# Optimization experiments

Measured on AMD Instinct MI355X. Metric: run time of the kernel, lower is better.

The kernel has to match this reference:

```python
import jax, jax.numpy as jnp
import numpy as np

N = 100000   # nodes
E = 1600000  # edges
D = 128      # feature dim
G = 64       # graphs in batch


def setup_inputs() -> dict:
    key = jax.random.key(0)
    k1, k2, k3, k4, k5, k6, k7, k8 = jax.random.split(key, 8)
    in_feat = jax.random.normal(k1, (N, D), dtype=jnp.float32)
    src = jax.random.randint(k2, (E,), 0, N, dtype=jnp.int32)
    dst = jax.random.randint(k3, (E,), 0, N, dtype=jnp.int32)
    graph_ids = jax.random.randint(k4, (N,), 0, G, dtype=jnp.int32)
    s = 1.0 / np.sqrt(D)
    W1 = jax.random.uniform(k5, (D, D), jnp.float32, -s, s)
    b1 = jnp.zeros((D,), jnp.float32)
    W2 = jax.random.uniform(k6, (D, D), jnp.float32, -s, s)
    b2 = jnp.zeros((D,), jnp.float32)
    return {"in_feat": in_feat, "W1": W1, "b1": b1, "W2": W2, "b2": b2,
            "src": src, "dst": dst, "graph_ids": graph_ids}


def _graph_conv(x, src, dst, W, b, norm_src, norm_dst):
    # DGL GraphConv, norm='both': D_out^{-1/2} A D_in^{-1/2} X W + b
    m = (x * norm_src[:, None])[src]                       # [E, d] gather
    agg = jax.ops.segment_sum(m, dst, num_segments=N)      # [N, d] scatter-add
    return (agg * norm_dst[:, None]) @ W + b


def reference(in_feat, W1, b1, W2, b2, src, dst, graph_ids):
    ones_e = jnp.ones((E,), jnp.float32)
    deg_out = jax.ops.segment_sum(ones_e, src, num_segments=N)
    deg_in = jax.ops.segment_sum(ones_e, dst, num_segments=N)
    norm_src = jnp.where(deg_out > 0, deg_out, 1.0) ** -0.5  # D_out^{-1/2}
    norm_dst = jnp.where(deg_in > 0, deg_in, 1.0) ** -0.5    # D_in^{-1/2}

    h = _graph_conv(in_feat, src, dst, W1, b1, norm_src, norm_dst)
    h = jax.nn.relu(h)
    h = _graph_conv(h, src, dst, W2, b2, norm_src, norm_dst)

    # AvgPooling: per-graph mean over nodes -> [G, D]
    sums = jax.ops.segment_sum(h, graph_ids, num_segments=G)
    counts = jax.ops.segment_sum(jnp.ones((N,), jnp.float32), graph_ids, num_segments=G)
    return sums / jnp.maximum(counts, 1.0)[:, None]
```

## Files before the change

kernel.cpp:

```cpp
#include <hip/hip_runtime.h>
#include <cstdint>


#define DD 128
#define PB 512
#define GB 384
#define KC 32
#define CHK 3200

typedef __attribute__((ext_vector_type(8))) short bf16x8;
typedef __attribute__((ext_vector_type(4))) float f32x4;
typedef __attribute__((ext_vector_type(2))) float f32x2;

__device__ __forceinline__ unsigned short f2bf(float f) {
  union { float f; unsigned u; } v; v.f = f;
  unsigned r = (v.u + 0x7fff + ((v.u >> 16) & 1)) >> 16;
  return (unsigned short)r;
}
__device__ __forceinline__ unsigned cvt_pk_bf16(float lo, float hi) {
  unsigned r;
  asm("v_cvt_pk_bf16_f32 %0, %1, %2" : "=v"(r) : "v"(lo), "v"(hi));
  return r;
}
__device__ __forceinline__ unsigned char f2fp8(float f) {
  return (unsigned char)(__builtin_amdgcn_cvt_pk_fp8_f32(f, f, 0, false) & 0xff);
}

__global__ __launch_bounds__(256) void k_part1a(const int* __restrict__ src, const int* __restrict__ dst,
                                                const int* __restrict__ gid,
                                                unsigned* __restrict__ histD, unsigned* __restrict__ histS,
                                                unsigned* __restrict__ rawD, unsigned* __restrict__ rawS,
                                                int* __restrict__ gcnt,
                                                const float* __restrict__ W1, unsigned short* __restrict__ Wt,
                                                unsigned char* __restrict__ zrow,
                                                int E, int N, int G) {
  if (blockIdx.x >= PB) {
    int wb = blockIdx.x - PB;
    int n = wb * 2 + (threadIdx.x >> 7), k = threadIdx.x & 127;
    Wt[n * 128 + k] = f2bf(W1[k * 128 + n]);
    if (wb == 0 && threadIdx.x < 128) zrow[threadIdx.x] = 0;
    return;
  }
  __shared__ unsigned hD[256], hS[256];
  __shared__ int h64[64];
  hD[threadIdx.x] = 0; hS[threadIdx.x] = 0;
  if (threadIdx.x < 64) h64[threadIdx.x] = 0;
  __syncthreads();
  int chunk = (E + PB - 1) / PB;
  int e0 = blockIdx.x * chunk, e1 = min(E, e0 + chunk);
  for (int e = e0 + threadIdx.x; e < e1; e += 256) {
    atomicAdd(&hD[(unsigned)dst[e] >> 9], 1u);
    atomicAdd(&hS[(unsigned)src[e] >> 9], 1u);
  }
  int stride = PB * 256;
  for (int i = blockIdx.x * 256 + threadIdx.x; i < N; i += stride)
    atomicAdd(&h64[gid[i]], 1);
  __syncthreads();
  unsigned vd = hD[threadIdx.x], vs = hS[threadIdx.x];
  histD[blockIdx.x * 256 + threadIdx.x] = vd;
  histS[blockIdx.x * 256 + threadIdx.x] = vs;
  rawD[blockIdx.x * 256 + threadIdx.x] = vd;
  rawS[blockIdx.x * 256 + threadIdx.x] = vs;
  if (threadIdx.x < (unsigned)G) {
    int v = h64[threadIdx.x];
    if (v) atomicAdd(&gcnt[threadIdx.x], v);
  }
}

__global__ __launch_bounds__(256) void k_pscanA(unsigned* __restrict__ histD, unsigned* __restrict__ histS,
                                                unsigned* __restrict__ tot) {
  __shared__ unsigned excl[PB], psc[256];
  int table = blockIdx.x >> 8, b = blockIdx.x & 255;
  unsigned* hist = table ? histS : histD;
  int t = threadIdx.x;
  unsigned s0 = hist[(2 * t) * 256 + b];
  unsigned s1 = hist[(2 * t + 1) * 256 + b];
  unsigned pr = s0 + s1;
  psc[t] = pr;
  __syncthreads();
  for (int off = 1; off < 256; off <<= 1) {
    unsigned x = (t >= off) ? psc[t - off] : 0;
    __syncthreads();
    psc[t] += x;
    __syncthreads();
  }
  unsigned pex = psc[t] - pr;
  excl[2 * t] = pex;
  excl[2 * t + 1] = pex + s0;
  __syncthreads();
  hist[(2 * t) * 256 + b] = excl[2 * t];
  hist[(2 * t + 1) * 256 + b] = excl[2 * t + 1];
  if (t == 255) tot[table * 256 + b] = psc[255];
}

__global__ __launch_bounds__(256) void k_pscanB(const unsigned* __restrict__ tot,
                                                int* __restrict__ bsD, int* __restrict__ bsS) {
  __shared__ unsigned s[256];
  int t = threadIdx.x;
#pragma unroll
  for (int table = 0; table < 2; ++table) {
    int* bs = table ? bsS : bsD;
    unsigned v = tot[table * 256 + t];
    s[t] = v;
    __syncthreads();
    for (int off = 1; off < 256; off <<= 1) {
      unsigned x = (t >= off) ? s[t - off] : 0;
      __syncthreads();
      s[t] += x;
      __syncthreads();
    }
    bs[t] = (int)(s[t] - v);
    if (t == 255) bs[256] = (int)s[255];
    __syncthreads();
  }
}

__global__ __launch_bounds__(256) void k_part1c(const int* __restrict__ src, const int* __restrict__ dst,
                                                const unsigned* __restrict__ histD, const unsigned* __restrict__ histS,
                                                const unsigned* __restrict__ rawD, const unsigned* __restrict__ rawS,
                                                const int* __restrict__ bsD, const int* __restrict__ bsS,
                                                unsigned* __restrict__ pairD, unsigned* __restrict__ pairS, int E) {
  __shared__ unsigned pkD[CHK], pkS[CHK];
  __shared__ unsigned char bkD[CHK], bkS[CHK];
  __shared__ unsigned curD[256], curS[256], gbD[256], gbS[256], psc[256];
  int chunk = (E + gridDim.x - 1) / gridDim.x;
  int e0 = blockIdx.x * chunk, e1 = min(E, e0 + chunk);
  int n = e1 - e0;
  int t = threadIdx.x;
  unsigned vD = rawD[blockIdx.x * 256 + t];
  psc[t] = vD;
  __syncthreads();
  for (int off = 1; off < 256; off <<= 1) {
    unsigned x = (t >= off) ? psc[t - off] : 0;
    __syncthreads();
    psc[t] += x;
    __syncthreads();
  }
  unsigned exD = psc[t] - vD;
  curD[t] = exD;
  gbD[t] = histD[blockIdx.x * 256 + t] + (unsigned)bsD[t] - exD;
  __syncthreads();
  unsigned vS = rawS[blockIdx.x * 256 + t];
  psc[t] = vS;
  __syncthreads();
  for (int off = 1; off < 256; off <<= 1) {
    unsigned x = (t >= off) ? psc[t - off] : 0;
    __syncthreads();
    psc[t] += x;
    __syncthreads();
  }
  unsigned exS = psc[t] - vS;
  curS[t] = exS;
  gbS[t] = histS[blockIdx.x * 256 + t] + (unsigned)bsS[t] - exS;
  __syncthreads();
  for (int i = t; i < n; i += 256) {
    unsigned sv = (unsigned)src[e0 + i], dv = (unsigned)dst[e0 + i];
    unsigned bD = dv >> 9, bS = sv >> 9;
    unsigned pD = atomicAdd(&curD[bD], 1u);
    pkD[pD] = ((dv & 511u) << 17) | sv;
    bkD[pD] = (unsigned char)bD;
    unsigned pS = atomicAdd(&curS[bS], 1u);
    pkS[pS] = ((sv & 511u) << 17) | dv;
    bkS[pS] = (unsigned char)bS;
  }
  __syncthreads();
  for (int i = t; i < n; i += 256)
    pairD[gbD[bkD[i]] + i] = pkD[i];
  for (int i = t; i < n; i += 256)
    pairS[gbS[bkS[i]] + i] = pkS[i];
}

__global__ __launch_bounds__(256) void k_part2d(const unsigned* __restrict__ pairD, const int* __restrict__ bsD,
                                                const int* __restrict__ gcnt, const int* __restrict__ gid,
                                                int* __restrict__ offs, float* __restrict__ ndst,
                                                uint2* __restrict__ pwg, int* __restrict__ degI,
                                                int* __restrict__ dbin,
                                                int* __restrict__ srcS, int N) {
  __shared__ unsigned hist[512], excl[512], psc[256];
  __shared__ int ldb[256];
  int k = blockIdx.x, base = k << 9;
  int b0 = bsD[k], b1 = bsD[k + 1];
  hist[threadIdx.x] = 0; hist[threadIdx.x + 256] = 0;
  ldb[threadIdx.x] = 0;
  __syncthreads();
  for (int i = b0 + threadIdx.x; i < b1; i += 256)
    atomicAdd(&hist[pairD[i] >> 17], 1u);
  __syncthreads();
  unsigned s0 = hist[2 * threadIdx.x], s1 = hist[2 * threadIdx.x + 1];
  unsigned pr = s0 + s1;
  psc[threadIdx.x] = pr;
  __syncthreads();
  for (int off = 1; off < 256; off <<= 1) {
    unsigned x = (threadIdx.x >= off) ? psc[threadIdx.x - off] : 0;
    __syncthreads();
    psc[threadIdx.x] += x;
    __syncthreads();
  }
  unsigned pex = psc[threadIdx.x] - pr;
  excl[2 * threadIdx.x] = pex;
  excl[2 * threadIdx.x + 1] = pex + s0;
  __syncthreads();
  for (int j = threadIdx.x; j < 512; j += 256) {
    int node = base + j;
    if (node <= N) offs[node] = b0 + (int)excl[j];
    if (node < N) {
      int dg = (int)hist[j];
      degI[node] = dg;
      atomicAdd(&ldb[255 - min(dg, 255)], 1);
      float gi = (float)dg; gi = gi > 0.f ? gi : 1.f;
      float nd = rsqrtf(gi);
      ndst[node] = nd;
      float c = (float)gcnt[gid[node]]; c = c > 1.f ? c : 1.f;
      float w = nd / c;
      union { float f; unsigned u; } v; v.f = w;
      pwg[node] = make_uint2(v.u, (unsigned)gid[node]);
    }
  }
  __syncthreads();
  if (ldb[threadIdx.x]) atomicAdd(&dbin[threadIdx.x], ldb[threadIdx.x]);
  for (int i = b0 + threadIdx.x; i < b1; i += 256) {
    unsigned pkv = pairD[i];
    unsigned pos = atomicAdd(&excl[pkv >> 17], 1u);
    srcS[b0 + (int)pos] = (int)(pkv & 0x1FFFFu);
  }
}

__global__ __launch_bounds__(256) void k_dscan(const int* __restrict__ dbin, int* __restrict__ dcur) {
  __shared__ int s[256];
  int t = threadIdx.x;
  int v = dbin[t];
  s[t] = v;
  __syncthreads();
  for (int off = 1; off < 256; off <<= 1) {
    int x = (t >= off) ? s[t - off] : 0;
    __syncthreads();
    s[t] += x;
    __syncthreads();
  }
  dcur[t] = s[t] - v;
}

__global__ __launch_bounds__(256) void k_dperm(const int* __restrict__ degI, int* __restrict__ dcur,
                                               int* __restrict__ perm, int N) {
  __shared__ int lh[256], lcur[256];
  int t = threadIdx.x, i = blockIdx.x * 256 + t;
  lh[t] = 0;
  __syncthreads();
  int bin = 0;
  if (i < N) {
    bin = 255 - min(degI[i], 255);
    atomicAdd(&lh[bin], 1);
  }
  __syncthreads();
  int r = lh[t] ? atomicAdd(&dcur[t], lh[t]) : 0;
  lcur[t] = r;
  __syncthreads();
  if (i < N) {
    int pos = atomicAdd(&lcur[bin], 1);
    perm[pos] = i;
  }
}

__global__ __launch_bounds__(1024, 1) void k_pw(const unsigned* __restrict__ pairS, const int* __restrict__ bsS,
                                                const uint2* __restrict__ pwg,
                                                unsigned short* __restrict__ P16,
                                                float* __restrict__ nsrc, int N) {
  __shared__ float tile[512 * 64];
  __shared__ unsigned hist[512];
  int k = blockIdx.x, base = k << 9;
  int b0 = bsS[k], b1 = bsS[k + 1];
  for (int i = threadIdx.x; i < 512 * 64; i += 1024) tile[i] = 0.f;
  if (threadIdx.x < 512) hist[threadIdx.x] = 0;
  __syncthreads();
  for (int i = b0 + threadIdx.x; i < b1; i += 1024) {
    unsigned pkv = pairS[i];
    unsigned dv = pkv & 0x1FFFFu;
    unsigned sloc = pkv >> 17;
    atomicAdd(&hist[sloc], 1u);
    uint2 u = pwg[dv];
    union { unsigned u; float f; } w; w.u = u.x;
    atomicAdd(&tile[sloc * 64 + u.y], w.f);
  }
  __syncthreads();
  if (threadIdx.x < 512) {
    int node = base + threadIdx.x;
    if (node < N) {
      float g = (float)hist[threadIdx.x]; g = g > 0.f ? g : 1.f;
      nsrc[node] = rsqrtf(g);
    }
  }
  for (int grp = threadIdx.x; grp < 4096; grp += 1024) {
    int qb = grp >> 6, g = grp & 63;
    unsigned w0 = cvt_pk_bf16(tile[(qb * 8 + 0) * 64 + g], tile[(qb * 8 + 1) * 64 + g]);
    unsigned w1 = cvt_pk_bf16(tile[(qb * 8 + 2) * 64 + g], tile[(qb * 8 + 3) * 64 + g]);
    unsigned w2 = cvt_pk_bf16(tile[(qb * 8 + 4) * 64 + g], tile[(qb * 8 + 5) * 64 + g]);
    unsigned w3 = cvt_pk_bf16(tile[(qb * 8 + 6) * 64 + g], tile[(qb * 8 + 7) * 64 + g]);
    uint4 o = make_uint4(w0, w1, w2, w3);
    *(uint4*)(P16 + ((size_t)(base >> 3) + qb) * 512 + g * 8) = o;
  }
}

__global__ __launch_bounds__(512) void k_gemm1(const float* __restrict__ X, const unsigned short* __restrict__ Wt,
                                               const float* __restrict__ nsrc,
                                               unsigned char* __restrict__ Z8, int N) {
  __shared__ unsigned short Wl[128 * 128];
  int wave = threadIdx.x >> 6, lane = threadIdx.x & 63;
  int quad = lane >> 4, l16 = lane & 15;
  int row0 = blockIdx.x * 128 + wave * 16;
  int arow = row0 + l16; if (arow >= N) arow = N - 1;
  const float* xr = X + (size_t)arow * 128 + quad * 8;
  float4 xv[8];
#pragma unroll
  for (int kbi = 0; kbi < 4; ++kbi) {
    xv[2 * kbi]     = *(const float4*)(xr + kbi * 32);
    xv[2 * kbi + 1] = *(const float4*)(xr + kbi * 32 + 4);
  }
  int rbase = row0 + quad * 4;
  float sc[4];
#pragma unroll
  for (int r = 0; r < 4; ++r) {
    int row = rbase + r; if (row >= N) row = N - 1;
    sc[r] = nsrc[row];
  }
  for (int i = threadIdx.x; i < 2048; i += 512) {
    int wrow = i >> 4, sgrp = i & 15;
    *(uint4*)(Wl + wrow * 128 + ((sgrp ^ (wrow & 15)) << 3)) = ((const uint4*)Wt)[i];
  }
  __syncthreads();
  f32x4 acc[8];
#pragma unroll
  for (int i = 0; i < 8; ++i) acc[i] = (f32x4){0.f, 0.f, 0.f, 0.f};
#pragma unroll
  for (int kbi = 0; kbi < 4; ++kbi) {
    float4 x0 = xv[2 * kbi], x1 = xv[2 * kbi + 1];
    union { unsigned u[4]; bf16x8 v; } A;
    A.u[0] = cvt_pk_bf16(x0.x, x0.y);
    A.u[1] = cvt_pk_bf16(x0.z, x0.w);
    A.u[2] = cvt_pk_bf16(x1.x, x1.y);
    A.u[3] = cvt_pk_bf16(x1.z, x1.w);
#pragma unroll
    for (int nt = 0; nt < 8; ++nt) {
      bf16x8 b = *(const bf16x8*)(Wl + (nt * 16 + l16) * 128 + (((kbi * 4 + quad) ^ l16) << 3));
      acc[nt] = __builtin_amdgcn_mfma_f32_16x16x32_bf16(A.v, b, acc[nt], 0, 0, 0);
    }
  }
#pragma unroll
  for (int r = 0; r < 4; ++r) {
    int row = rbase + r;
    if (row < N) {
      float s = sc[r];
#pragma unroll
      for (int nt = 0; nt < 8; ++nt)
        Z8[(size_t)row * 128 + nt * 16 + l16] = f2fp8(acc[nt][r] * s);
    }
  }
}

#define ACC16(u) do {                                             \
    c0 += __builtin_amdgcn_cvt_pk_f32_fp8((u).x, false);          \
    c1 += __builtin_amdgcn_cvt_pk_f32_fp8((u).x, true);           \
    c2 += __builtin_amdgcn_cvt_pk_f32_fp8((u).y, false);          \
    c3 += __builtin_amdgcn_cvt_pk_f32_fp8((u).y, true);           \
    c4 += __builtin_amdgcn_cvt_pk_f32_fp8((u).z, false);          \
    c5 += __builtin_amdgcn_cvt_pk_f32_fp8((u).z, true);           \
    c6 += __builtin_amdgcn_cvt_pk_f32_fp8((u).w, false);          \
    c7 += __builtin_amdgcn_cvt_pk_f32_fp8((u).w, true);           \
  } while (0)

__global__ __launch_bounds__(256) void k_layer1(const unsigned char* __restrict__ Z8,
                                                const int* __restrict__ offs, const int* __restrict__ srcS,
                                                const int* __restrict__ perm,
                                                const float* __restrict__ b1,
                                                const float* __restrict__ nsrc, const float* __restrict__ ndst,
                                                unsigned short* __restrict__ Hb, int N) {
  int lane = threadIdx.x & 63;
  int oct = lane >> 3, l8 = lane & 7;
  const int f = l8 * 16;
  const unsigned char* zb = Z8 + f;
  int gstride = gridDim.x * 32;
  for (int base = blockIdx.x * 32; base < N; base += gstride) {
    int dd = base + (threadIdx.x >> 6) * 8 + oct;
    bool live = dd < N;
    int pd = perm[live ? dd : 0];
    int start = offs[pd];
    int end = live ? offs[pd + 1] : start;
    float nd = ndst[pd], ns = nsrc[pd];
    f32x2 c0 = {0.f, 0.f}, c1 = {0.f, 0.f}, c2 = {0.f, 0.f}, c3 = {0.f, 0.f};
    f32x2 c4 = {0.f, 0.f}, c5 = {0.f, 0.f}, c6 = {0.f, 0.f}, c7 = {0.f, 0.f};
    int e = start;
    int rem = end - start;
    int s0 = N, s1 = N, s2 = N, s3 = N;
    if (rem > 0) s0 = srcS[e];
    if (rem > 1) s1 = srcS[e + 1];
    if (rem > 2) s2 = srcS[e + 2];
    if (rem > 3) s3 = srcS[e + 3];
    while (__any(rem > 0)) {
      uint4 u0 = *(const uint4*)(zb + ((size_t)s0 << 7));
      uint4 u1 = *(const uint4*)(zb + ((size_t)s1 << 7));
      uint4 u2 = *(const uint4*)(zb + ((size_t)s2 << 7));
      uint4 u3 = *(const uint4*)(zb + ((size_t)s3 << 7));
      int n0 = N, n1 = N, n2 = N, n3 = N;
      if (rem > 4) n0 = srcS[e + 4];
      if (rem > 5) n1 = srcS[e + 5];
      if (rem > 6) n2 = srcS[e + 6];
      if (rem > 7) n3 = srcS[e + 7];
      ACC16(u0);
      ACC16(u1);
      ACC16(u2);
      ACC16(u3);
      s0 = n0; s1 = n1; s2 = n2; s3 = n3;
      e += 4;
      rem -= 4;
    }
    if (live) {
      float4 bv0 = *(const float4*)(b1 + f);
      float4 bv1 = *(const float4*)(b1 + f + 4);
      float4 bv2 = *(const float4*)(b1 + f + 8);
      float4 bv3 = *(const float4*)(b1 + f + 12);
      float h0 = fmaxf(fmaf(nd, c0[0], bv0.x), 0.f) * ns;
      float h1 = fmaxf(fmaf(nd, c0[1], bv0.y), 0.f) * ns;
      float h2 = fmaxf(fmaf(nd, c1[0], bv0.z), 0.f) * ns;
      float h3 = fmaxf(fmaf(nd, c1[1], bv0.w), 0.f) * ns;
      float h4 = fmaxf(fmaf(nd, c2[0], bv1.x), 0.f) * ns;
      float h5 = fmaxf(fmaf(nd, c2[1], bv1.y), 0.f) * ns;
      float h6 = fmaxf(fmaf(nd, c3[0], bv1.z), 0.f) * ns;
      float h7 = fmaxf(fmaf(nd, c3[1], bv1.w), 0.f) * ns;
      float h8 = fmaxf(fmaf(nd, c4[0], bv2.x), 0.f) * ns;
      float h9 = fmaxf(fmaf(nd, c4[1], bv2.y), 0.f) * ns;
      float hA = fmaxf(fmaf(nd, c5[0], bv2.z), 0.f) * ns;
      float hB = fmaxf(fmaf(nd, c5[1], bv2.w), 0.f) * ns;
      float hC = fmaxf(fmaf(nd, c6[0], bv3.x), 0.f) * ns;
      float hD = fmaxf(fmaf(nd, c6[1], bv3.y), 0.f) * ns;
      float hE = fmaxf(fmaf(nd, c7[0], bv3.z), 0.f) * ns;
      float hF = fmaxf(fmaf(nd, c7[1], bv3.w), 0.f) * ns;
      unsigned short* hrow = Hb + (size_t)pd * 128 + f;
      *(uint4*)hrow = make_uint4(cvt_pk_bf16(h0, h1), cvt_pk_bf16(h2, h3),
                                 cvt_pk_bf16(h4, h5), cvt_pk_bf16(h6, h7));
      *(uint4*)(hrow + 8) = make_uint4(cvt_pk_bf16(h8, h9), cvt_pk_bf16(hA, hB),
                                       cvt_pk_bf16(hC, hD), cvt_pk_bf16(hE, hF));
    }
  }
}

__global__ __launch_bounds__(256) void k_poolgemm(const unsigned short* __restrict__ P16,
                                                  const unsigned short* __restrict__ Hb,
                                                  float* __restrict__ pooled, int N, int Kpad, int chunk) {
  __shared__ unsigned short Hl[KC * 128];
  int t = threadIdx.x;
  int r0 = blockIdx.x * chunk;
  int r1 = min(Kpad, r0 + chunk);
  int wv = t >> 6, lane = t & 63, quad = lane >> 4, l16 = lane & 15;
  f32x4 acc[8];
#pragma unroll
  for (int i = 0; i < 8; ++i) acc[i] = (f32x4){0.f, 0.f, 0.f, 0.f};
  for (int rb = r0; rb < r1; rb += KC) {
    int r = t >> 3, c = (t & 7) * 16;
    int cs = c ^ ((r >> 3) * 16);
    int row = rb + r;
    if (row < N) {
      const uint4* srcp = (const uint4*)(Hb + (size_t)row * 128 + c);
      *(uint4*)(Hl + r * 128 + cs) = srcp[0];
      *(uint4*)(Hl + r * 128 + cs + 8) = srcp[1];
    } else {
      uint4 z = make_uint4(0, 0, 0, 0);
      *(uint4*)(Hl + r * 128 + cs) = z;
      *(uint4*)(Hl + r * 128 + cs + 8) = z;
    }
    __syncthreads();
    bf16x8 a = *(const bf16x8*)(P16 + ((size_t)(rb >> 3) + quad) * 512 + (wv * 16 + l16) * 8);
#pragma unroll
    for (int ft = 0; ft < 8; ++ft) {
      bf16x8 b;
#pragma unroll
      for (int j = 0; j < 8; ++j) {
        int rr = quad * 8 + j;
        b[j] = (short)Hl[rr * 128 + ((ft ^ (rr >> 3)) * 16) + l16];
      }
      acc[ft] = __builtin_amdgcn_mfma_f32_16x16x32_bf16(a, b, acc[ft], 0, 0, 0);
    }
    __syncthreads();
  }
#pragma unroll
  for (int ft = 0; ft < 8; ++ft)
#pragma unroll
    for (int rg = 0; rg < 4; ++rg)
      unsafeAtomicAdd(&pooled[(wv * 16 + quad * 4 + rg) * DD + ft * 16 + l16], acc[ft][rg]);
}

__global__ __launch_bounds__(128) void k_out(const float* __restrict__ pooled, const float* __restrict__ W2,
                                             const float* __restrict__ b2, float* __restrict__ out) {
  __shared__ float p[DD];
  int g = blockIdx.x, d = threadIdx.x;
  p[d] = pooled[g * DD + d];
  __syncthreads();
  float a = b2[d];
#pragma unroll 4
  for (int k = 0; k < DD; ++k) a = fmaf(p[k], W2[k * DD + d], a);
  out[g * DD + d] = a;
}

extern "C" void kernel_launch(void* const* d_in, const int* in_sizes, int n_in,
                              void* d_out, int out_size, void* d_ws, size_t ws_size,
                              hipStream_t stream) {
  const float* X  = (const float*)d_in[0];
  const float* W1 = (const float*)d_in[1];
  const float* b1 = (const float*)d_in[2];
  const float* W2 = (const float*)d_in[3];
  const float* b2 = (const float*)d_in[4];
  const int* src  = (const int*)d_in[5];
  const int* dst  = (const int*)d_in[6];
  const int* gid  = (const int*)d_in[7];
  int E = in_sizes[5];
  int N = in_sizes[7];
  int G = out_size / DD;
  int nb = (N >> 9) + 1;
  int Kpad = nb << 9;
  int chunk = ((Kpad + GB * KC - 1) / (GB * KC)) * KC;

  char* w = (char*)d_ws;
  size_t o = 0;
  auto carve = [&](size_t bytes) { char* p = w + o; o += (bytes + 255) & ~(size_t)255; return p; };
  int*   gcnt   = (int*)  carve((size_t)G * 4);
  float* pooled = (float*)carve((size_t)G * DD * 4);
  int*   dbin   = (int*)  carve(256 * 4);
  size_t zeroBytes = o;
  unsigned* histD = (unsigned*)carve((size_t)PB * 256 * 4);
  unsigned* histS = (unsigned*)carve((size_t)PB * 256 * 4);
  unsigned* rawD  = (unsigned*)carve((size_t)PB * 256 * 4);
  unsigned* rawS  = (unsigned*)carve((size_t)PB * 256 * 4);
  unsigned* tot   = (unsigned*)carve(512 * 4);
  int*   bsD    = (int*)  carve(257 * 4);
  int*   bsS    = (int*)  carve(257 * 4);
  int*   dcur   = (int*)  carve(256 * 4);
  unsigned* pairD = (unsigned*)carve((size_t)E * 4);
  unsigned* pairS = (unsigned*)carve((size_t)E * 4);
  int*   srcS   = (int*)  carve((size_t)E * 4);
  int*   offs   = (int*)  carve((size_t)(N + 1) * 4);
  int*   degI   = (int*)  carve((size_t)N * 4);
  int*   perm   = (int*)  carve((size_t)N * 4);
  float* nsrc   = (float*)carve((size_t)N * 4);
  float* ndst   = (float*)carve((size_t)N * 4);
  uint2* pwg    = (uint2*)carve((size_t)N * 8);
  unsigned short* Wt = (unsigned short*)carve(128 * 128 * 2);
  unsigned char*  Z8 = (unsigned char*)carve((size_t)(N + 1) * DD);
  unsigned short* Hb = (unsigned short*)carve((size_t)N * DD * 2);
  unsigned short* P16 = (unsigned short*)carve((size_t)Kpad * 64 * 2);

  hipMemsetAsync(d_ws, 0, zeroBytes, stream);

  k_part1a<<<PB + 64, 256, 0, stream>>>(src, dst, gid, histD, histS, rawD, rawS, gcnt,
                                        W1, Wt, Z8 + (size_t)N * DD, E, N, G);
  k_pscanA<<<512, 256, 0, stream>>>(histD, histS, tot);
  k_pscanB<<<1, 256, 0, stream>>>(tot, bsD, bsS);
  k_part1c<<<PB, 256, 0, stream>>>(src, dst, histD, histS, rawD, rawS, bsD, bsS, pairD, pairS, E);
  k_part2d<<<nb, 256, 0, stream>>>(pairD, bsD, gcnt, gid, offs, ndst, pwg, degI, dbin, srcS, N);
  k_dscan<<<1, 256, 0, stream>>>(dbin, dcur);
  k_dperm<<<(N + 255) / 256, 256, 0, stream>>>(degI, dcur, perm, N);
  k_pw<<<nb, 1024, 0, stream>>>(pairS, bsS, pwg, P16, nsrc, N);
  k_gemm1<<<(N + 127) / 128, 512, 0, stream>>>(X, Wt, nsrc, Z8, N);
  k_layer1<<<1024, 256, 0, stream>>>(Z8, offs, srcS, perm, b1, nsrc, ndst, Hb, N);
  k_poolgemm<<<GB, 256, 0, stream>>>(P16, Hb, pooled, N, Kpad, chunk);
  k_out<<<G, DD, 0, stream>>>(pooled, W2, b2, (float*)d_out);
}
```

Measured before the change: 272.3 us.

## Drop partition prefix-scan kernels, fuse degree scan, double-tile gemm1, widen layer1 grid

Removes the per-block column prefix-scan kernel by having each histogram block atomically accumulate bucket totals, with the scatter kernel claiming its global base through atomic adds on per-bucket cursors. The single-block degree-bin scan is folded into the degree permutation kernel, so every block recomputes the 256-bin scan itself. gemm1 now processes two 128-row tiles per block to amortise loading W into LDS, and layer1 launches twice as many blocks. Together these cut kernel launches and the hist traffic. In exchange the bucket ordering inside each bucket becomes nondeterministic across blocks, and global atomics contend on 256 counters.

```diff
diff --git a/kernel.cpp b/kernel.cpp
--- a/kernel.cpp
+++ b/kernel.cpp
@@ -28,8 +28,8 @@
 
 __global__ __launch_bounds__(256) void k_part1a(const int* __restrict__ src, const int* __restrict__ dst,
                                                 const int* __restrict__ gid,
-                                                unsigned* __restrict__ histD, unsigned* __restrict__ histS,
                                                 unsigned* __restrict__ rawD, unsigned* __restrict__ rawS,
+                                                unsigned* __restrict__ tot,
                                                 int* __restrict__ gcnt,
                                                 const float* __restrict__ W1, unsigned short* __restrict__ Wt,
                                                 unsigned char* __restrict__ zrow,
@@ -57,49 +57,25 @@
     atomicAdd(&h64[gid[i]], 1);
   __syncthreads();
   unsigned vd = hD[threadIdx.x], vs = hS[threadIdx.x];
-  histD[blockIdx.x * 256 + threadIdx.x] = vd;
-  histS[blockIdx.x * 256 + threadIdx.x] = vs;
   rawD[blockIdx.x * 256 + threadIdx.x] = vd;
   rawS[blockIdx.x * 256 + threadIdx.x] = vs;
+  if (vd) atomicAdd(&tot[threadIdx.x], vd);
+  if (vs) atomicAdd(&tot[256 + threadIdx.x], vs);
   if (threadIdx.x < (unsigned)G) {
     int v = h64[threadIdx.x];
     if (v) atomicAdd(&gcnt[threadIdx.x], v);
   }
 }
 
-__global__ __launch_bounds__(256) void k_pscanA(unsigned* __restrict__ histD, unsigned* __restrict__ histS,
-                                                unsigned* __restrict__ tot) {
-  __shared__ unsigned excl[PB], psc[256];
-  int table = blockIdx.x >> 8, b = blockIdx.x & 255;
-  unsigned* hist = table ? histS : histD;
-  int t = threadIdx.x;
-  unsigned s0 = hist[(2 * t) * 256 + b];
-  unsigned s1 = hist[(2 * t + 1) * 256 + b];
-  unsigned pr = s0 + s1;
-  psc[t] = pr;
-  __syncthreads();
-  for (int off = 1; off < 256; off <<= 1) {
-    unsigned x = (t >= off) ? psc[t - off] : 0;
-    __syncthreads();
-    psc[t] += x;
-    __syncthreads();
-  }
-  unsigned pex = psc[t] - pr;
-  excl[2 * t] = pex;
-  excl[2 * t + 1] = pex + s0;
-  __syncthreads();
-  hist[(2 * t) * 256 + b] = excl[2 * t];
-  hist[(2 * t + 1) * 256 + b] = excl[2 * t + 1];
-  if (t == 255) tot[table * 256 + b] = psc[255];
-}
-
 __global__ __launch_bounds__(256) void k_pscanB(const unsigned* __restrict__ tot,
-                                                int* __restrict__ bsD, int* __restrict__ bsS) {
+                                                int* __restrict__ bsD, int* __restrict__ bsS,
+                                                unsigned* __restrict__ curD, unsigned* __restrict__ curS) {
   __shared__ unsigned s[256];
   int t = threadIdx.x;
 #pragma unroll
   for (int table = 0; table < 2; ++table) {
     int* bs = table ? bsS : bsD;
+    unsigned* cur = table ? curS : curD;
     unsigned v = tot[table * 256 + t];
     s[t] = v;
     __syncthreads();
@@ -109,25 +85,27 @@
       s[t] += x;
       __syncthreads();
     }
-    bs[t] = (int)(s[t] - v);
+    unsigned e = s[t] - v;
+    bs[t] = (int)e;
+    cur[t] = e;
     if (t == 255) bs[256] = (int)s[255];
     __syncthreads();
   }
 }
 
 __global__ __launch_bounds__(256) void k_part1c(const int* __restrict__ src, const int* __restrict__ dst,
-                                                const unsigned* __restrict__ histD, const unsigned* __restrict__ histS,
                                                 const unsigned* __restrict__ rawD, const unsigned* __restrict__ rawS,
-                                                const int* __restrict__ bsD, const int* __restrict__ bsS,
+                                                unsigned* __restrict__ curDg, unsigned* __restrict__ curSg,
                                                 unsigned* __restrict__ pairD, unsigned* __restrict__ pairS, int E) {
   __shared__ unsigned pkD[CHK], pkS[CHK];
   __shared__ unsigned char bkD[CHK], bkS[CHK];
-  __shared__ unsigned curD[256], curS[256], gbD[256], gbS[256], psc[256];
+  __shared__ unsigned cD[256], cS[256], gbD[256], gbS[256], psc[256];
   int chunk = (E + gridDim.x - 1) / gridDim.x;
   int e0 = blockIdx.x * chunk, e1 = min(E, e0 + chunk);
   int n = e1 - e0;
   int t = threadIdx.x;
   unsigned vD = rawD[blockIdx.x * 256 + t];
+  unsigned baseD = atomicAdd(&curDg[t], vD);
   psc[t] = vD;
   __syncthreads();
   for (int off = 1; off < 256; off <<= 1) {
@@ -137,10 +115,11 @@
     __syncthreads();
   }
   unsigned exD = psc[t] - vD;
-  curD[t] = exD;
-  gbD[t] = histD[blockIdx.x * 256 + t] + (unsigned)bsD[t] - exD;
+  cD[t] = exD;
+  gbD[t] = baseD - exD;
   __syncthreads();
   unsigned vS = rawS[blockIdx.x * 256 + t];
+  unsigned baseS = atomicAdd(&curSg[t], vS);
   psc[t] = vS;
   __syncthreads();
   for (int off = 1; off < 256; off <<= 1) {
@@ -150,16 +129,16 @@
     __syncthreads();
   }
   unsigned exS = psc[t] - vS;
-  curS[t] = exS;
-  gbS[t] = histS[blockIdx.x * 256 + t] + (unsigned)bsS[t] - exS;
+  cS[t] = exS;
+  gbS[t] = baseS - exS;
   __syncthreads();
   for (int i = t; i < n; i += 256) {
     unsigned sv = (unsigned)src[e0 + i], dv = (unsigned)dst[e0 + i];
     unsigned bD = dv >> 9, bS = sv >> 9;
-    unsigned pD = atomicAdd(&curD[bD], 1u);
+    unsigned pD = atomicAdd(&cD[bD], 1u);
     pkD[pD] = ((dv & 511u) << 17) | sv;
     bkD[pD] = (unsigned char)bD;
-    unsigned pS = atomicAdd(&curS[bS], 1u);
+    unsigned pS = atomicAdd(&cS[bS], 1u);
     pkS[pS] = ((sv & 511u) << 17) | dv;
     bkS[pS] = (unsigned char)bS;
   }
@@ -225,11 +204,14 @@
   }
 }
 
-__global__ __launch_bounds__(256) void k_dscan(const int* __restrict__ dbin, int* __restrict__ dcur) {
-  __shared__ int s[256];
-  int t = threadIdx.x;
+__global__ __launch_bounds__(256) void k_dperm(const int* __restrict__ degI, const int* __restrict__ dbin,
+                                               int* __restrict__ dcur,
+                                               int* __restrict__ perm, int N) {
+  __shared__ int s[256], lh[256], lcur[256];
+  int t = threadIdx.x, i = blockIdx.x * 256 + t;
   int v = dbin[t];
   s[t] = v;
+  lh[t] = 0;
   __syncthreads();
   for (int off = 1; off < 256; off <<= 1) {
     int x = (t >= off) ? s[t - off] : 0;
@@ -237,15 +219,7 @@
     s[t] += x;
     __syncthreads();
   }
-  dcur[t] = s[t] - v;
-}
-
-__global__ __launch_bounds__(256) void k_dperm(const int* __restrict__ degI, int* __restrict__ dcur,
-                                               int* __restrict__ perm, int N) {
-  __shared__ int lh[256], lcur[256];
-  int t = threadIdx.x, i = blockIdx.x * 256 + t;
-  lh[t] = 0;
-  __syncthreads();
+  int excl = s[t] - v;
   int bin = 0;
   if (i < N) {
     bin = 255 - min(degI[i], 255);
@@ -253,7 +227,7 @@
   }
   __syncthreads();
   int r = lh[t] ? atomicAdd(&dcur[t], lh[t]) : 0;
-  lcur[t] = r;
+  lcur[t] = excl + r;
   __syncthreads();
   if (i < N) {
     int pos = atomicAdd(&lcur[bin], 1);
@@ -302,25 +276,34 @@
 
 __global__ __launch_bounds__(512) void k_gemm1(const float* __restrict__ X, const unsigned short* __restrict__ Wt,
                                                const float* __restrict__ nsrc,
-                                               unsigned char* __restrict__ Z8, int N) {
+                                               unsigned char* __restrict__ Z8, int N, int ntiles) {
   __shared__ unsigned short Wl[128 * 128];
   int wave = threadIdx.x >> 6, lane = threadIdx.x & 63;
   int quad = lane >> 4, l16 = lane & 15;
-  int row0 = blockIdx.x * 128 + wave * 16;
-  int arow = row0 + l16; if (arow >= N) arow = N - 1;
-  const float* xr = X + (size_t)arow * 128 + quad * 8;
-  float4 xv[8];
+  int t0 = blockIdx.x * 2, t1 = t0 + 1;
+  bool has1 = t1 < ntiles;
+  int row0a = t0 * 128 + wave * 16;
+  int row0b = t1 * 128 + wave * 16;
+  int arowa = row0a + l16; if (arowa >= N) arowa = N - 1;
+  int arowb = row0b + l16; if (arowb >= N) arowb = N - 1;
+  const float* xra = X + (size_t)arowa * 128 + quad * 8;
+  const float* xrb = X + (size_t)arowb * 128 + quad * 8;
+  float4 xa[8], xb[8];
 #pragma unroll
   for (int kbi = 0; kbi < 4; ++kbi) {
-    xv[2 * kbi]     = *(const float4*)(xr + kbi * 32);
-    xv[2 * kbi + 1] = *(const float4*)(xr + kbi * 32 + 4);
-  }
-  int rbase = row0 + quad * 4;
-  float sc[4];
+    xa[2 * kbi]     = *(const float4*)(xra + kbi * 32);
+    xa[2 * kbi + 1] = *(const float4*)(xra + kbi * 32 + 4);
+    xb[2 * kbi]     = *(const float4*)(xrb + kbi * 32);
+    xb[2 * kbi + 1] = *(const float4*)(xrb + kbi * 32 + 4);
+  }
+  int rbasea = row0a + quad * 4, rbaseb = row0b + quad * 4;
+  float sca[4], scb[4];
 #pragma unroll
   for (int r = 0; r < 4; ++r) {
-    int row = rbase + r; if (row >= N) row = N - 1;
-    sc[r] = nsrc[row];
+    int ra = rbasea + r; if (ra >= N) ra = N - 1;
+    int rb = rbaseb + r; if (rb >= N) rb = N - 1;
+    sca[r] = nsrc[ra];
+    scb[r] = nsrc[rb];
   }
   for (int i = threadIdx.x; i < 2048; i += 512) {
     int wrow = i >> 4, sgrp = i & 15;
@@ -332,7 +315,7 @@
   for (int i = 0; i < 8; ++i) acc[i] = (f32x4){0.f, 0.f, 0.f, 0.f};
 #pragma unroll
   for (int kbi = 0; kbi < 4; ++kbi) {
-    float4 x0 = xv[2 * kbi], x1 = xv[2 * kbi + 1];
+    float4 x0 = xa[2 * kbi], x1 = xa[2 * kbi + 1];
     union { unsigned u[4]; bf16x8 v; } A;
     A.u[0] = cvt_pk_bf16(x0.x, x0.y);
     A.u[1] = cvt_pk_bf16(x0.z, x0.w);
@@ -346,9 +329,36 @@
   }
 #pragma unroll
   for (int r = 0; r < 4; ++r) {
-    int row = rbase + r;
+    int row = rbasea + r;
     if (row < N) {
-      float s = sc[r];
+      float s = sca[r];
+#pragma unroll
+      for (int nt = 0; nt < 8; ++nt)
+        Z8[(size_t)row * 128 + nt * 16 + l16] = f2fp8(acc[nt][r] * s);
+    }
+  }
+  if (!has1) return;
+#pragma unroll
+  for (int i = 0; i < 8; ++i) acc[i] = (f32x4){0.f, 0.f, 0.f, 0.f};
+#pragma unroll
+  for (int kbi = 0; kbi < 4; ++kbi) {
+    float4 x0 = xb[2 * kbi], x1 = xb[2 * kbi + 1];
+    union { unsigned u[4]; bf16x8 v; } A;
+    A.u[0] = cvt_pk_bf16(x0.x, x0.y);
+    A.u[1] = cvt_pk_bf16(x0.z, x0.w);
+    A.u[2] = cvt_pk_bf16(x1.x, x1.y);
+    A.u[3] = cvt_pk_bf16(x1.z, x1.w);
+#pragma unroll
+    for (int nt = 0; nt < 8; ++nt) {
+      bf16x8 b = *(const bf16x8*)(Wl + (nt * 16 + l16) * 128 + (((kbi * 4 + quad) ^ l16) << 3));
+      acc[nt] = __builtin_amdgcn_mfma_f32_16x16x32_bf16(A.v, b, acc[nt], 0, 0, 0);
+    }
+  }
+#pragma unroll
+  for (int r = 0; r < 4; ++r) {
+    int row = rbaseb + r;
+    if (row < N) {
+      float s = scb[r];
 #pragma unroll
       for (int nt = 0; nt < 8; ++nt)
         Z8[(size_t)row * 128 + nt * 16 + l16] = f2fp8(acc[nt][r] * s);
@@ -516,6 +526,7 @@
   int nb = (N >> 9) + 1;
   int Kpad = nb << 9;
   int chunk = ((Kpad + GB * KC - 1) / (GB * KC)) * KC;
+  int ntiles = (N + 127) / 128;
 
   char* w = (char*)d_ws;
   size_t o = 0;
@@ -523,15 +534,15 @@
   int*   gcnt   = (int*)  carve((size_t)G * 4);
   float* pooled = (float*)carve((size_t)G * DD * 4);
   int*   dbin   = (int*)  carve(256 * 4);
+  unsigned* tot = (unsigned*)carve(512 * 4);
+  int*   dcur   = (int*)  carve(256 * 4);
   size_t zeroBytes = o;
-  unsigned* histD = (unsigned*)carve((size_t)PB * 256 * 4);
-  unsigned* histS = (unsigned*)carve((size_t)PB * 256 * 4);
   unsigned* rawD  = (unsigned*)carve((size_t)PB * 256 * 4);
   unsigned* rawS  = (unsigned*)carve((size_t)PB * 256 * 4);
-  unsigned* tot   = (unsigned*)carve(512 * 4);
   int*   bsD    = (int*)  carve(257 * 4);
   int*   bsS    = (int*)  carve(257 * 4);
-  int*   dcur   = (int*)  carve(256 * 4);
+  unsigned* curD = (unsigned*)carve(256 * 4);
+  unsigned* curS = (unsigned*)carve(256 * 4);
   unsigned* pairD = (unsigned*)carve((size_t)E * 4);
   unsigned* pairS = (unsigned*)carve((size_t)E * 4);
   int*   srcS   = (int*)  carve((size_t)E * 4);
@@ -548,17 +559,15 @@
 
   hipMemsetAsync(d_ws, 0, zeroBytes, stream);
 
-  k_part1a<<<PB + 64, 256, 0, stream>>>(src, dst, gid, histD, histS, rawD, rawS, gcnt,
+  k_part1a<<<PB + 64, 256, 0, stream>>>(src, dst, gid, rawD, rawS, tot, gcnt,
                                         W1, Wt, Z8 + (size_t)N * DD, E, N, G);
-  k_pscanA<<<512, 256, 0, stream>>>(histD, histS, tot);
-  k_pscanB<<<1, 256, 0, stream>>>(tot, bsD, bsS);
-  k_part1c<<<PB, 256, 0, stream>>>(src, dst, histD, histS, rawD, rawS, bsD, bsS, pairD, pairS, E);
+  k_pscanB<<<1, 256, 0, stream>>>(tot, bsD, bsS, curD, curS);
+  k_part1c<<<PB, 256, 0, stream>>>(src, dst, rawD, rawS, curD, curS, pairD, pairS, E);
   k_part2d<<<nb, 256, 0, stream>>>(pairD, bsD, gcnt, gid, offs, ndst, pwg, degI, dbin, srcS, N);
-  k_dscan<<<1, 256, 0, stream>>>(dbin, dcur);
-  k_dperm<<<(N + 255) / 256, 256, 0, stream>>>(degI, dcur, perm, N);
+  k_dperm<<<(N + 255) / 256, 256, 0, stream>>>(degI, dbin, dcur, perm, N);
   k_pw<<<nb, 1024, 0, stream>>>(pairS, bsS, pwg, P16, nsrc, N);
-  k_gemm1<<<(N + 127) / 128, 512, 0, stream>>>(X, Wt, nsrc, Z8, N);
-  k_layer1<<<1024, 256, 0, stream>>>(Z8, offs, srcS, perm, b1, nsrc, ndst, Hb, N);
+  k_gemm1<<<(ntiles + 1) / 2, 512, 0, stream>>>(X, Wt, nsrc, Z8, N, ntiles);
+  k_layer1<<<2048, 256, 0, stream>>>(Z8, offs, srcS, perm, b1, nsrc, ndst, Hb, N);
   k_poolgemm<<<GB, 256, 0, stream>>>(P16, Hb, pooled, N, Kpad, chunk);
   k_out<<<G, DD, 0, stream>>>(pooled, W2, b2, (float*)d_out);
 }
```

After: 277.7 us. About the same (+2.0%).
